# Performance work log

Measured on AMD Instinct MI355X. Metric: run time of the kernel, lower is better.

Reference implementation:

```python
import jax, jax.numpy as jnp
import numpy as np

BN_EPS = 1e-5
KEEP_RATIO = 0.25
MIN_TOPK = 4


def setup_inputs() -> dict:
    key = jax.random.key(0)
    ks = jax.random.split(key, 8)
    B, C, H, W, HID = 32, 768, 32, 32, 96
    x = jax.random.normal(ks[0], (B, C, H, W), dtype=jnp.float32)
    # fan-in scaled weights so score magnitudes stay sane for softmax
    w1 = jax.random.normal(ks[1], (HID, C, 1, 1), dtype=jnp.float32) / np.sqrt(C)
    bn_gamma = jax.random.uniform(ks[2], (HID,), dtype=jnp.float32) + 0.5
    bn_beta = jax.random.normal(ks[3], (HID,), dtype=jnp.float32) * 0.1
    bn_mean = jax.random.normal(ks[4], (HID,), dtype=jnp.float32) * 0.1
    bn_var = jax.random.uniform(ks[5], (HID,), dtype=jnp.float32) + 0.5
    w2 = jax.random.normal(ks[6], (1, HID, 3, 3), dtype=jnp.float32) / np.sqrt(HID * 9)
    b2 = jax.random.normal(ks[7], (1,), dtype=jnp.float32) * 0.1
    return {"x": x, "w1": w1, "bn_gamma": bn_gamma, "bn_beta": bn_beta,
            "bn_mean": bn_mean, "bn_var": bn_var, "w2": w2, "b2": b2}


def reference(x, w1, bn_gamma, bn_beta, bn_mean, bn_var, w2, b2):
    B, C, H, W = x.shape
    N = H * W
    # 1x1 conv (no bias) as channel contraction: [B,C,H,W] x [HID,C] -> [B,HID,H,W]
    h = jnp.einsum('bchw,oc->bohw', x, w1[:, :, 0, 0])
    # BatchNorm in inference mode (running stats)
    scale = (bn_gamma / jnp.sqrt(bn_var + BN_EPS))[None, :, None, None]
    h = h * scale + (bn_beta - bn_mean * bn_gamma / jnp.sqrt(bn_var + BN_EPS))[None, :, None, None]
    h = jax.nn.relu(h)
    # 3x3 conv HID -> 1, padding=1
    score = jax.lax.conv_general_dilated(
        h, w2, window_strides=(1, 1), padding='SAME',
        dimension_numbers=('NCHW', 'OIHW', 'NCHW')) + b2[None, :, None, None]
    s = score.reshape(B, N)
    K = min(max(MIN_TOPK, int(N * KEEP_RATIO)), N)
    top_vals, top_idx = jax.lax.top_k(s, K)  # [B,K] (sorted; weighted sum is order-invariant)
    x_flat = x.reshape(B, C, N)
    sel = jnp.take_along_axis(x_flat, top_idx[:, None, :], axis=2)  # [B,C,K]
    w = jax.nn.softmax(top_vals, axis=1)[:, None, :]               # [B,1,K]
    v = jnp.sum(sel * w, axis=2)                                    # [B,C]
    # dropout p=0.0 -> identity
    return v, score.reshape(B, 1, H, W)
```

## Files before the change

### kernel.cpp

```cpp
#include <hip/hip_runtime.h>
#include <math.h>

#define BB 32
#define CC 768
#define HID 96
#define NPIX 1024
#define KSEL 256
#define BN_EPS_F 1e-5f

typedef __bf16 bf16x8 __attribute__((ext_vector_type(8)));
typedef float f32x4 __attribute__((ext_vector_type(4)));

__device__ __forceinline__ unsigned short f2bf(float f) {
    unsigned u = __float_as_uint(f);
    return (unsigned short)((u + 0x7FFFu + ((u >> 16) & 1u)) >> 16);
}
__device__ __forceinline__ unsigned pack2(float lo, float hi) {
    return (unsigned)f2bf(lo) | ((unsigned)f2bf(hi) << 16);
}

__global__ __launch_bounds__(512, 4) void k1_gemm_mfma(
    const float* __restrict__ x, const float* __restrict__ w1,
    const float* __restrict__ gamma, const float* __restrict__ beta,
    const float* __restrict__ mean, const float* __restrict__ var,
    float* __restrict__ h_out)
{
    constexpr int WSTR = 388;
    __shared__ unsigned short Ws[96 * WSTR];
    __shared__ float sc_s[HID], sh_s[HID];

    const int t = threadIdx.x;
    const int b = blockIdx.y;
    const int n0 = blockIdx.x * 64;
    const int wave = t >> 6, lane = t & 63;
    const int lm = lane & 15, g = lane >> 4;
    const int wo = wave & 1, wn = wave >> 1;
    const int n = n0 + wn * 16 + lm;

    if (t < HID) {
        float sc = gamma[t] * rsqrtf(var[t] + BN_EPS_F);
        sc_s[t] = sc;
        sh_s[t] = beta[t] - mean[t] * sc;
    }

    f32x4 acc[3];
#pragma unroll
    for (int mt = 0; mt < 3; ++mt) acc[mt] = (f32x4){0.f, 0.f, 0.f, 0.f};

    const float* xcol = x + (size_t)b * CC * NPIX + (size_t)(g * 8) * NPIX + n;

#define STAGE_W(half) do {                                                    \
    _Pragma("unroll")                                                         \
    for (int i = 0; i < 9; ++i) {                                             \
        int idx = t + i * 512;                                   \
        int row = idx / 48, k8 = (idx % 48) * 8;                              \
        const float* src = w1 + (size_t)row * CC + (half) * 384 + k8;         \
        float4 f0 = *reinterpret_cast<const float4*>(src);                    \
        float4 f1 = *reinterpret_cast<const float4*>(src + 4);                \
        uint4 o;                                                              \
        o.x = pack2(f0.x, f0.y); o.y = pack2(f0.z, f0.w);                     \
        o.z = pack2(f1.x, f1.y); o.w = pack2(f1.z, f1.w);                     \
        *reinterpret_cast<uint4*>(&Ws[row * WSTR + k8]) = o;                  \
    } } while (0)

#define LOADX(dst, ck) do {                                                   \
    const float* _p = xcol + (size_t)(ck) * 32 * NPIX;                        \
    _Pragma("unroll")                                                         \
    for (int j = 0; j < 8; ++j) dst[j] = _p[(size_t)j * NPIX];                \
    } while (0)

#define PACKX(bu, src) do {                                                   \
    bu.x = pack2(src[0], src[1]); bu.y = pack2(src[2], src[3]);               \
    bu.z = pack2(src[4], src[5]); bu.w = pack2(src[6], src[7]); } while (0)

#define CHUNK(ckk, bu) do {                                                   \
    bf16x8 bfr = __builtin_bit_cast(bf16x8, bu);                              \
    _Pragma("unroll")                                                         \
    for (int mt = 0; mt < 3; ++mt) {                                          \
        uint4 au = *reinterpret_cast<const uint4*>(                           \
            &Ws[(wo * 48 + mt * 16 + lm) * WSTR + (ckk) * 32 + g * 8]);       \
        acc[mt] = __builtin_amdgcn_mfma_f32_16x16x32_bf16(                    \
            __builtin_bit_cast(bf16x8, au), bfr, acc[mt], 0, 0, 0);           \
    } } while (0)

    float xA[8], xB[8], xC[8], xD[8];

    STAGE_W(0);
    LOADX(xA, 0); LOADX(xB, 1); LOADX(xC, 2); LOADX(xD, 3);
    __syncthreads();

#pragma unroll
    for (int ck = 0; ck < 24; ck += 4) {
        if (ck == 12) {
            __syncthreads();
            STAGE_W(1);
            __syncthreads();
        }
        uint4 bu0; PACKX(bu0, xA);
        if (ck + 4 < 24) LOADX(xA, ck + 4);
        CHUNK((ck + 0) % 12, bu0);

        uint4 bu1; PACKX(bu1, xB);
        if (ck + 5 < 24) LOADX(xB, ck + 5);
        CHUNK((ck + 1) % 12, bu1);

        uint4 bu2; PACKX(bu2, xC);
        if (ck + 6 < 24) LOADX(xC, ck + 6);
        CHUNK((ck + 2) % 12, bu2);

        uint4 bu3; PACKX(bu3, xD);
        if (ck + 7 < 24) LOADX(xD, ck + 7);
        CHUNK((ck + 3) % 12, bu3);
    }

#pragma unroll
    for (int mt = 0; mt < 3; ++mt) {
#pragma unroll
        for (int r = 0; r < 4; ++r) {
            int o = wo * 48 + mt * 16 + g * 4 + r;
            float v = fmaxf(acc[mt][r] * sc_s[o] + sh_s[o], 0.f);
            h_out[((size_t)b * HID + o) * NPIX + n] = v;
        }
    }
#undef STAGE_W
#undef LOADX
#undef PACKX
#undef CHUNK
}

__global__ __launch_bounds__(128) void k2_conv3x3(
    const float* __restrict__ h_in, const float* __restrict__ w2,
    const float* __restrict__ b2, float* __restrict__ score_out)
{
    __shared__ float hs[16][6][40];
    __shared__ float w2s[HID * 9];

    const int t = threadIdx.x;
    const int ytile = blockIdx.x, b = blockIdx.y;
    const int y = t >> 5, xx = t & 31;
    const int Y = ytile * 4 + y;

    for (int i = t; i < HID * 9; i += 128) w2s[i] = w2[i];

    const float* hb = h_in + (size_t)b * HID * NPIX;
    float acc = 0.f;

    for (int c0 = 0; c0 < HID; c0 += 16) {
        __syncthreads();
        for (int i = t; i < 192; i += 128) {
            int ch = i / 12, rr = (i % 12) >> 1, col = (i & 1) ? 36 : 3;
            hs[ch][rr][col] = 0.f;
        }
#pragma unroll
        for (int i = 0; i < 6; ++i) {
            int idx = t + i * 128;
            int ch = idx / 48, rem = idx % 48;
            int rr = rem >> 3, qq = rem & 7;
            int gy = ytile * 4 - 1 + rr;
            float4 v = (gy >= 0 && gy < 32)
                ? *reinterpret_cast<const float4*>(
                      hb + (size_t)(c0 + ch) * NPIX + gy * 32 + qq * 4)
                : (float4){0.f, 0.f, 0.f, 0.f};
            *reinterpret_cast<float4*>(&hs[ch][rr][4 + qq * 4]) = v;
        }
        __syncthreads();
#pragma unroll
        for (int ch = 0; ch < 16; ++ch) {
            float s = 0.f;
#pragma unroll
            for (int ky = 0; ky < 3; ++ky)
#pragma unroll
                for (int kx = 0; kx < 3; ++kx)
                    s += hs[ch][y + ky][3 + xx + kx] * w2s[(c0 + ch) * 9 + ky * 3 + kx];
            acc += s;
        }
    }
    score_out[b * NPIX + Y * 32 + xx] = acc + b2[0];
}

__global__ __launch_bounds__(256) void k3_topk_softmax(
    const float* __restrict__ score, float* __restrict__ weight)
{
    __shared__ unsigned hist[256];
    __shared__ unsigned wtot[4];
    __shared__ unsigned pcnt16[16];
    __shared__ float redf[4];
    __shared__ unsigned sh_bin, sh_rem;

    const int t = threadIdx.x, b = blockIdx.x;
    const int lane = t & 63, wv = t >> 6;

    float fvals[4];
    unsigned uvals[4];
#pragma unroll
    for (int i = 0; i < 4; ++i) {
        float f = score[b * NPIX + t + 256 * i];
        fvals[i] = f;
        unsigned u = __float_as_uint(f);
        uvals[i] = (u & 0x80000000u) ? ~u : (u | 0x80000000u);
    }

    unsigned prefix = 0, rem = KSEL;
    for (int p = 3; p >= 0; --p) {
        hist[t] = 0;
        __syncthreads();
        const int sh_hi = (p + 1) * 8;
#pragma unroll
        for (int i = 0; i < 4; ++i) {
            unsigned u = uvals[i];
            bool match = (p == 3) || ((u >> sh_hi) == (prefix >> sh_hi));
            if (match) atomicAdd(&hist[(u >> (p * 8)) & 0xffu], 1u);
        }
        __syncthreads();
        unsigned own = hist[t];
        unsigned val = own;
#pragma unroll
        for (int off = 1; off <= 32; off <<= 1) {
            unsigned o2 = __shfl_down(val, off);
            if (lane + off < 64) val += o2;
        }
        if (lane == 0) wtot[wv] = val;
        __syncthreads();
        unsigned suff = val;
        for (int w = wv + 1; w < 4; ++w) suff += wtot[w];
        unsigned nexts = suff - own;
        if (suff >= rem && nexts < rem) { sh_bin = (unsigned)t; sh_rem = rem - nexts; }
        __syncthreads();
        prefix |= (sh_bin << (p * 8));
        rem = sh_rem;
        __syncthreads();
    }
    const unsigned T = prefix, need = rem;

    float m = -INFINITY;
#pragma unroll
    for (int i = 0; i < 4; ++i) m = fmaxf(m, fvals[i]);
#pragma unroll
    for (int off = 32; off >= 1; off >>= 1) m = fmaxf(m, __shfl_xor(m, off));
    if (lane == 0) redf[wv] = m;
    __syncthreads();
    m = fmaxf(fmaxf(redf[0], redf[1]), fmaxf(redf[2], redf[3]));

    unsigned lp[4]; bool eqf[4], gtf[4];
    unsigned long long lmask = (1ULL << lane) - 1ULL;
#pragma unroll
    for (int i = 0; i < 4; ++i) {
        bool eq = (uvals[i] == T);
        eqf[i] = eq; gtf[i] = (uvals[i] > T);
        unsigned long long mk = __ballot(eq);
        lp[i] = (unsigned)__popcll(mk & lmask);
        if (lane == 0) pcnt16[i * 4 + wv] = (unsigned)__popcll(mk);
    }
    __syncthreads();
    unsigned cum = 0, baseArr[4];
#pragma unroll
    for (int ii = 0; ii < 4; ++ii) {
        unsigned b0 = cum;
        for (int w = 0; w < wv; ++w) b0 += pcnt16[ii * 4 + w];
        baseArr[ii] = b0;
        for (int w = 0; w < 4; ++w) cum += pcnt16[ii * 4 + w];
    }
    float evals[4], sumExp = 0.f;
#pragma unroll
    for (int i = 0; i < 4; ++i) {
        bool sel = gtf[i] || (eqf[i] && (baseArr[i] + lp[i]) < need);
        float e = sel ? expf(fvals[i] - m) : 0.f;
        evals[i] = e;
        sumExp += e;
    }
#pragma unroll
    for (int off = 32; off >= 1; off >>= 1) sumExp += __shfl_xor(sumExp, off);
    if (lane == 0) redf[wv] = sumExp;
    __syncthreads();
    float inv = 1.0f / (redf[0] + redf[1] + redf[2] + redf[3]);
#pragma unroll
    for (int i = 0; i < 4; ++i)
        weight[b * NPIX + i * 256 + t] = evals[i] * inv;
}

__global__ __launch_bounds__(256) void k4_weighted_sum(
    const float* __restrict__ x, const float* __restrict__ weight,
    float* __restrict__ v)
{
    __shared__ float wsm[NPIX];
    const int t = threadIdx.x;
    const int b = blockIdx.x / 192, cg = blockIdx.x % 192;

    *reinterpret_cast<float4*>(&wsm[t * 4]) =
        *reinterpret_cast<const float4*>(&weight[b * NPIX + t * 4]);
    __syncthreads();

    const int lane = t & 63, wvv = t >> 6;
    const int c = cg * 4 + wvv;
    const float* xr = x + ((size_t)b * CC + c) * NPIX;

    float acc = 0.f;
#pragma unroll
    for (int j = 0; j < 4; ++j) {
        int off = j * 256 + lane * 4;
        float4 xv = *reinterpret_cast<const float4*>(xr + off);
        float4 wv4 = *reinterpret_cast<const float4*>(&wsm[off]);
        acc += xv.x * wv4.x + xv.y * wv4.y + xv.z * wv4.z + xv.w * wv4.w;
    }
#pragma unroll
    for (int off = 32; off >= 1; off >>= 1) acc += __shfl_xor(acc, off);
    if (lane == 0) v[(size_t)b * CC + c] = acc;
}

extern "C" void kernel_launch(void* const* d_in, const int* in_sizes, int n_in,
                              void* d_out, int out_size, void* d_ws, size_t ws_size,
                              hipStream_t stream)
{
    const float* x     = (const float*)d_in[0];
    const float* w1    = (const float*)d_in[1];
    const float* gamma = (const float*)d_in[2];
    const float* beta  = (const float*)d_in[3];
    const float* mean  = (const float*)d_in[4];
    const float* var   = (const float*)d_in[5];
    const float* w2    = (const float*)d_in[6];
    const float* b2    = (const float*)d_in[7];

    float* out   = (float*)d_out;
    float* vout  = out;
    float* score = out + BB * CC;

    float* h      = (float*)d_ws;
    float* weight = h + (size_t)BB * HID * NPIX;

    k1_gemm_mfma<<<dim3(16, BB), 512, 0, stream>>>(x, w1, gamma, beta, mean, var, h);
    k2_conv3x3<<<dim3(8, BB), 128, 0, stream>>>(h, w2, b2, score);
    k3_topk_softmax<<<BB, 256, 0, stream>>>(score, weight);
    k4_weighted_sum<<<BB * (CC / 4), 256, 0, stream>>>(x, weight, vout);
}
```

Measured before the change: 74.43 us.

## Widen GEMM tile to 128 pixels with float2 x loads and dual MFMA accumulators

The 1x1-conv GEMM kernel now covers 128 pixels per block instead of 64. Each lane loads adjacent pixel pairs as float2 and feeds two MFMA accumulator sets, so every bf16 weight fragment read from shared memory is reused twice. This halves the number of blocks and the redundant staging of W1 into LDS per block, and widens the global loads and stores. In exchange it uses more registers per thread, lowers the launch-bounds occupancy hint from 4 to 2, and leaves fewer blocks (256) to spread across the CUs.

```diff
diff --git a/kernel.cpp b/kernel.cpp
--- a/kernel.cpp
+++ b/kernel.cpp
@@ -19,7 +19,7 @@
     return (unsigned)f2bf(lo) | ((unsigned)f2bf(hi) << 16);
 }
 
-__global__ __launch_bounds__(512, 4) void k1_gemm_mfma(
+__global__ __launch_bounds__(512, 2) void k1_gemm_mfma(
     const float* __restrict__ x, const float* __restrict__ w1,
     const float* __restrict__ gamma, const float* __restrict__ beta,
     const float* __restrict__ mean, const float* __restrict__ var,
@@ -31,11 +31,12 @@
 
     const int t = threadIdx.x;
     const int b = blockIdx.y;
-    const int n0 = blockIdx.x * 64;
+    const int n0 = blockIdx.x * 128;
     const int wave = t >> 6, lane = t & 63;
     const int lm = lane & 15, g = lane >> 4;
-    const int wo = wave & 1, wn = wave >> 1;
-    const int n = n0 + wn * 16 + lm;
+    const int wo = wave >> 2, wn = wave & 3;
+    const int nw = n0 + wn * 32;
+    const int ncol = nw + 2 * lm;
 
     if (t < HID) {
         float sc = gamma[t] * rsqrtf(var[t] + BN_EPS_F);
@@ -43,11 +44,14 @@
         sh_s[t] = beta[t] - mean[t] * sc;
     }
 
-    f32x4 acc[3];
-#pragma unroll
-    for (int mt = 0; mt < 3; ++mt) acc[mt] = (f32x4){0.f, 0.f, 0.f, 0.f};
-
-    const float* xcol = x + (size_t)b * CC * NPIX + (size_t)(g * 8) * NPIX + n;
+    f32x4 acc0[3], acc1[3];
+#pragma unroll
+    for (int mt = 0; mt < 3; ++mt) {
+        acc0[mt] = (f32x4){0.f, 0.f, 0.f, 0.f};
+        acc1[mt] = (f32x4){0.f, 0.f, 0.f, 0.f};
+    }
+
+    const float* xcol = x + (size_t)b * CC * NPIX + (size_t)(g * 8) * NPIX + ncol;
 
 #define STAGE_W(half) do {                                                    \
     _Pragma("unroll")                                                         \
@@ -66,24 +70,32 @@
 #define LOADX(dst, ck) do {                                                   \
     const float* _p = xcol + (size_t)(ck) * 32 * NPIX;                        \
     _Pragma("unroll")                                                         \
-    for (int j = 0; j < 8; ++j) dst[j] = _p[(size_t)j * NPIX];                \
+    for (int j = 0; j < 8; ++j)                                               \
+        dst[j] = *reinterpret_cast<const float2*>(_p + (size_t)j * NPIX);     \
     } while (0)
 
-#define PACKX(bu, src) do {                                                   \
-    bu.x = pack2(src[0], src[1]); bu.y = pack2(src[2], src[3]);               \
-    bu.z = pack2(src[4], src[5]); bu.w = pack2(src[6], src[7]); } while (0)
-
-#define CHUNK(ckk, bu) do {                                                   \
-    bf16x8 bfr = __builtin_bit_cast(bf16x8, bu);                              \
+#define PACKX(bu0, bu1, src) do {                                             \
+    bu0.x = pack2(src[0].x, src[1].x); bu0.y = pack2(src[2].x, src[3].x);     \
+    bu0.z = pack2(src[4].x, src[5].x); bu0.w = pack2(src[6].x, src[7].x);     \
+    bu1.x = pack2(src[0].y, src[1].y); bu1.y = pack2(src[2].y, src[3].y);     \
+    bu1.z = pack2(src[4].y, src[5].y); bu1.w = pack2(src[6].y, src[7].y);     \
+    } while (0)
+
+#define CHUNK(ckk, bu0, bu1) do {                                             \
+    bf16x8 bf0 = __builtin_bit_cast(bf16x8, bu0);                             \
+    bf16x8 bf1 = __builtin_bit_cast(bf16x8, bu1);                             \
     _Pragma("unroll")                                                         \
     for (int mt = 0; mt < 3; ++mt) {                                          \
         uint4 au = *reinterpret_cast<const uint4*>(                           \
             &Ws[(wo * 48 + mt * 16 + lm) * WSTR + (ckk) * 32 + g * 8]);       \
-        acc[mt] = __builtin_amdgcn_mfma_f32_16x16x32_bf16(                    \
-            __builtin_bit_cast(bf16x8, au), bfr, acc[mt], 0, 0, 0);           \
+        bf16x8 abf = __builtin_bit_cast(bf16x8, au);                          \
+        acc0[mt] = __builtin_amdgcn_mfma_f32_16x16x32_bf16(                   \
+            abf, bf0, acc0[mt], 0, 0, 0);                                     \
+        acc1[mt] = __builtin_amdgcn_mfma_f32_16x16x32_bf16(                   \
+            abf, bf1, acc1[mt], 0, 0, 0);                                     \
     } } while (0)
 
-    float xA[8], xB[8], xC[8], xD[8];
+    float2 xA[8], xB[8], xC[8], xD[8];
 
     STAGE_W(0);
     LOADX(xA, 0); LOADX(xB, 1); LOADX(xC, 2); LOADX(xD, 3);
@@ -96,21 +108,25 @@
             STAGE_W(1);
             __syncthreads();
         }
-        uint4 bu0; PACKX(bu0, xA);
+        uint4 p0, p1;
+        PACKX(p0, p1, xA);
         if (ck + 4 < 24) LOADX(xA, ck + 4);
-        CHUNK((ck + 0) % 12, bu0);
-
-        uint4 bu1; PACKX(bu1, xB);
+        CHUNK((ck + 0) % 12, p0, p1);
+
+        uint4 q0, q1;
+        PACKX(q0, q1, xB);
         if (ck + 5 < 24) LOADX(xB, ck + 5);
-        CHUNK((ck + 1) % 12, bu1);
-
-        uint4 bu2; PACKX(bu2, xC);
+        CHUNK((ck + 1) % 12, q0, q1);
+
+        uint4 r0, r1;
+        PACKX(r0, r1, xC);
         if (ck + 6 < 24) LOADX(xC, ck + 6);
-        CHUNK((ck + 2) % 12, bu2);
-
-        uint4 bu3; PACKX(bu3, xD);
+        CHUNK((ck + 2) % 12, r0, r1);
+
+        uint4 s0, s1;
+        PACKX(s0, s1, xD);
         if (ck + 7 < 24) LOADX(xD, ck + 7);
-        CHUNK((ck + 3) % 12, bu3);
+        CHUNK((ck + 3) % 12, s0, s1);
     }
 
 #pragma unroll
@@ -118,8 +134,12 @@
 #pragma unroll
         for (int r = 0; r < 4; ++r) {
             int o = wo * 48 + mt * 16 + g * 4 + r;
-            float v = fmaxf(acc[mt][r] * sc_s[o] + sh_s[o], 0.f);
-            h_out[((size_t)b * HID + o) * NPIX + n] = v;
+            float sc = sc_s[o], sh = sh_s[o];
+            float2 v;
+            v.x = fmaxf(acc0[mt][r] * sc + sh, 0.f);
+            v.y = fmaxf(acc1[mt][r] * sc + sh, 0.f);
+            *reinterpret_cast<float2*>(
+                &h_out[((size_t)b * HID + o) * NPIX + ncol]) = v;
         }
     }
 #undef STAGE_W
@@ -327,7 +347,7 @@
     float* h      = (float*)d_ws;
     float* weight = h + (size_t)BB * HID * NPIX;
 
-    k1_gemm_mfma<<<dim3(16, BB), 512, 0, stream>>>(x, w1, gamma, beta, mean, var, h);
+    k1_gemm_mfma<<<dim3(8, BB), 512, 0, stream>>>(x, w1, gamma, beta, mean, var, h);
     k2_conv3x3<<<dim3(8, BB), 128, 0, stream>>>(h, w2, b2, score);
     k3_topk_softmax<<<BB, 256, 0, stream>>>(score, weight);
     k4_weighted_sum<<<BB * (CC / 4), 256, 0, stream>>>(x, weight, vout);
```

Result: slower. 75.94 us (+2.0%).

## Split GEMM K dimension across two blocks and precompute bf16 weights

Applied to the files above, without the earlier changes.

Adds a prep kernel that converts w1 to bf16 once and computes BN scale/shift. The 1x1-conv GEMM is split into two K halves across a grid z dimension, each writing a partial result. The BN, ReLU and partial-sum reduction move into the conv3x3 load stage, and shared memory per GEMM block shrinks to allow higher occupancy. The aim is more parallelism and less per-block weight staging, at the cost of an extra kernel launch and twice the intermediate h traffic.

```diff
diff --git a/kernel.cpp b/kernel.cpp
--- a/kernel.cpp
+++ b/kernel.cpp
@@ -19,121 +19,126 @@
     return (unsigned)f2bf(lo) | ((unsigned)f2bf(hi) << 16);
 }
 
-__global__ __launch_bounds__(512, 4) void k1_gemm_mfma(
-    const float* __restrict__ x, const float* __restrict__ w1,
-    const float* __restrict__ gamma, const float* __restrict__ beta,
-    const float* __restrict__ mean, const float* __restrict__ var,
-    float* __restrict__ h_out)
-{
-    constexpr int WSTR = 388;
-    __shared__ unsigned short Ws[96 * WSTR];
-    __shared__ float sc_s[HID], sh_s[HID];
+__global__ __launch_bounds__(256) void k0_prep(
+    const float* __restrict__ w1, const float* __restrict__ gamma,
+    const float* __restrict__ beta, const float* __restrict__ mean,
+    const float* __restrict__ var,
+    unsigned short* __restrict__ w1b, float* __restrict__ scale,
+    float* __restrict__ shift)
+{
+    int t = threadIdx.x, bk = blockIdx.x;
+    if (bk < 72) {
+        int idx = (bk * 256 + t) * 4;
+        float4 v = *reinterpret_cast<const float4*>(w1 + idx);
+        uint2 o;
+        o.x = pack2(v.x, v.y);
+        o.y = pack2(v.z, v.w);
+        *reinterpret_cast<uint2*>(w1b + idx) = o;
+    } else if (t < HID) {
+        float sc = gamma[t] * rsqrtf(var[t] + BN_EPS_F);
+        scale[t] = sc;
+        shift[t] = beta[t] - mean[t] * sc;
+    }
+}
+
+__global__ __launch_bounds__(512, 6) void k1_gemm_mfma(
+    const float* __restrict__ x, const unsigned short* __restrict__ w1b,
+    float* __restrict__ h0, float* __restrict__ h1)
+{
+    __shared__ unsigned short Ws[96][100];
 
     const int t = threadIdx.x;
     const int b = blockIdx.y;
     const int n0 = blockIdx.x * 64;
+    const int kz = blockIdx.z;
+    const int kbase = kz * 384;
     const int wave = t >> 6, lane = t & 63;
     const int lm = lane & 15, g = lane >> 4;
-    const int wo = wave & 1, wn = wave >> 1;
+    const int wo = wave >> 2, wn = wave & 3;
     const int n = n0 + wn * 16 + lm;
 
-    if (t < HID) {
-        float sc = gamma[t] * rsqrtf(var[t] + BN_EPS_F);
-        sc_s[t] = sc;
-        sh_s[t] = beta[t] - mean[t] * sc;
-    }
-
     f32x4 acc[3];
 #pragma unroll
     for (int mt = 0; mt < 3; ++mt) acc[mt] = (f32x4){0.f, 0.f, 0.f, 0.f};
 
-    const float* xcol = x + (size_t)b * CC * NPIX + (size_t)(g * 8) * NPIX + n;
-
-#define STAGE_W(half) do {                                                    \
+    const float* xcol = x + (size_t)b * CC * NPIX
+                          + (size_t)(kbase + g * 8) * NPIX + n;
+
+#define STAGE_W(e) do {                                                       \
+    for (int ii = t; ii < 1152; ii += 512) {                                  \
+        int row = ii / 12, kc = (ii % 12) * 8;                                \
+        uint4 wv = *reinterpret_cast<const uint4*>(                           \
+            w1b + (size_t)row * CC + kbase + (e) * 96 + kc);                  \
+        *reinterpret_cast<uint4*>(&Ws[row][kc]) = wv;                         \
+    } } while (0)
+
+#define LOADX(dst, s) do {                                                    \
     _Pragma("unroll")                                                         \
-    for (int i = 0; i < 9; ++i) {                                             \
-        int idx = t + i * 512;                                   \
-        int row = idx / 48, k8 = (idx % 48) * 8;                              \
-        const float* src = w1 + (size_t)row * CC + (half) * 384 + k8;         \
-        float4 f0 = *reinterpret_cast<const float4*>(src);                    \
-        float4 f1 = *reinterpret_cast<const float4*>(src + 4);                \
-        uint4 o;                                                              \
-        o.x = pack2(f0.x, f0.y); o.y = pack2(f0.z, f0.w);                     \
-        o.z = pack2(f1.x, f1.y); o.w = pack2(f1.z, f1.w);                     \
-        *reinterpret_cast<uint4*>(&Ws[row * WSTR + k8]) = o;                  \
-    } } while (0)
-
-#define LOADX(dst, ck) do {                                                   \
-    const float* _p = xcol + (size_t)(ck) * 32 * NPIX;                        \
-    _Pragma("unroll")                                                         \
-    for (int j = 0; j < 8; ++j) dst[j] = _p[(size_t)j * NPIX];                \
+    for (int j = 0; j < 8; ++j)                                               \
+        dst[j] = xcol[(size_t)((s) * 32 + j) * NPIX];                         \
     } while (0)
 
 #define PACKX(bu, src) do {                                                   \
     bu.x = pack2(src[0], src[1]); bu.y = pack2(src[2], src[3]);               \
     bu.z = pack2(src[4], src[5]); bu.w = pack2(src[6], src[7]); } while (0)
 
-#define CHUNK(ckk, bu) do {                                                   \
+#define DOCHUNK(sl, bu) do {                                                  \
     bf16x8 bfr = __builtin_bit_cast(bf16x8, bu);                              \
     _Pragma("unroll")                                                         \
     for (int mt = 0; mt < 3; ++mt) {                                          \
         uint4 au = *reinterpret_cast<const uint4*>(                           \
-            &Ws[(wo * 48 + mt * 16 + lm) * WSTR + (ckk) * 32 + g * 8]);       \
+            &Ws[wo * 48 + mt * 16 + lm][(sl) * 32 + g * 8]);                  \
         acc[mt] = __builtin_amdgcn_mfma_f32_16x16x32_bf16(                    \
             __builtin_bit_cast(bf16x8, au), bfr, acc[mt], 0, 0, 0);           \
     } } while (0)
 
-    float xA[8], xB[8], xC[8], xD[8];
+#define STEP(sc, CUR) do {                                                    \
+    uint4 bu;                                                                 \
+    PACKX(bu, CUR);                                                           \
+    if ((sc) + 2 < 12) LOADX(CUR, (sc) + 2);                                  \
+    DOCHUNK((sc) % 3, bu);                                                    \
+    } while (0)
+
+    float xA[8], xB[8];
 
     STAGE_W(0);
-    LOADX(xA, 0); LOADX(xB, 1); LOADX(xC, 2); LOADX(xD, 3);
-    __syncthreads();
-
-#pragma unroll
-    for (int ck = 0; ck < 24; ck += 4) {
-        if (ck == 12) {
-            __syncthreads();
-            STAGE_W(1);
-            __syncthreads();
-        }
-        uint4 bu0; PACKX(bu0, xA);
-        if (ck + 4 < 24) LOADX(xA, ck + 4);
-        CHUNK((ck + 0) % 12, bu0);
-
-        uint4 bu1; PACKX(bu1, xB);
-        if (ck + 5 < 24) LOADX(xB, ck + 5);
-        CHUNK((ck + 1) % 12, bu1);
-
-        uint4 bu2; PACKX(bu2, xC);
-        if (ck + 6 < 24) LOADX(xC, ck + 6);
-        CHUNK((ck + 2) % 12, bu2);
-
-        uint4 bu3; PACKX(bu3, xD);
-        if (ck + 7 < 24) LOADX(xD, ck + 7);
-        CHUNK((ck + 3) % 12, bu3);
-    }
-
+    LOADX(xA, 0);
+    LOADX(xB, 1);
+    __syncthreads();
+
+    STEP(0, xA); STEP(1, xB); STEP(2, xA);
+    __syncthreads(); STAGE_W(1); __syncthreads();
+    STEP(3, xB); STEP(4, xA); STEP(5, xB);
+    __syncthreads(); STAGE_W(2); __syncthreads();
+    STEP(6, xA); STEP(7, xB); STEP(8, xA);
+    __syncthreads(); STAGE_W(3); __syncthreads();
+    STEP(9, xB); STEP(10, xA); STEP(11, xB);
+
+    float* hp = (kz == 0) ? h0 : h1;
 #pragma unroll
     for (int mt = 0; mt < 3; ++mt) {
 #pragma unroll
         for (int r = 0; r < 4; ++r) {
             int o = wo * 48 + mt * 16 + g * 4 + r;
-            float v = fmaxf(acc[mt][r] * sc_s[o] + sh_s[o], 0.f);
-            h_out[((size_t)b * HID + o) * NPIX + n] = v;
+            hp[((size_t)b * HID + o) * NPIX + n] = acc[mt][r];
         }
     }
 #undef STAGE_W
 #undef LOADX
 #undef PACKX
-#undef CHUNK
+#undef DOCHUNK
+#undef STEP
 }
 
 __global__ __launch_bounds__(128) void k2_conv3x3(
-    const float* __restrict__ h_in, const float* __restrict__ w2,
-    const float* __restrict__ b2, float* __restrict__ score_out)
+    const float* __restrict__ h0, const float* __restrict__ h1,
+    const float* __restrict__ scale, const float* __restrict__ shift,
+    const float* __restrict__ w2, const float* __restrict__ b2,
+    float* __restrict__ score_out)
 {
     __shared__ float hs[16][6][40];
     __shared__ float w2s[HID * 9];
+    __shared__ float sc_s[HID], sh_s[HID];
 
     const int t = threadIdx.x;
     const int ytile = blockIdx.x, b = blockIdx.y;
@@ -141,8 +146,10 @@
     const int Y = ytile * 4 + y;
 
     for (int i = t; i < HID * 9; i += 128) w2s[i] = w2[i];
-
-    const float* hb = h_in + (size_t)b * HID * NPIX;
+    if (t < HID) { sc_s[t] = scale[t]; sh_s[t] = shift[t]; }
+
+    const float* hb0 = h0 + (size_t)b * HID * NPIX;
+    const float* hb1 = h1 + (size_t)b * HID * NPIX;
     float acc = 0.f;
 
     for (int c0 = 0; c0 < HID; c0 += 16) {
@@ -157,10 +164,17 @@
             int ch = idx / 48, rem = idx % 48;
             int rr = rem >> 3, qq = rem & 7;
             int gy = ytile * 4 - 1 + rr;
-            float4 v = (gy >= 0 && gy < 32)
-                ? *reinterpret_cast<const float4*>(
-                      hb + (size_t)(c0 + ch) * NPIX + gy * 32 + qq * 4)
-                : (float4){0.f, 0.f, 0.f, 0.f};
+            float4 v = {0.f, 0.f, 0.f, 0.f};
+            if (gy >= 0 && gy < 32) {
+                size_t off = (size_t)(c0 + ch) * NPIX + gy * 32 + qq * 4;
+                float4 a = *reinterpret_cast<const float4*>(hb0 + off);
+                float4 c = *reinterpret_cast<const float4*>(hb1 + off);
+                float sc = sc_s[c0 + ch], sh = sh_s[c0 + ch];
+                v.x = fmaxf((a.x + c.x) * sc + sh, 0.f);
+                v.y = fmaxf((a.y + c.y) * sc + sh, 0.f);
+                v.z = fmaxf((a.z + c.z) * sc + sh, 0.f);
+                v.w = fmaxf((a.w + c.w) * sc + sh, 0.f);
+            }
             *reinterpret_cast<float4*>(&hs[ch][rr][4 + qq * 4]) = v;
         }
         __syncthreads();
@@ -324,11 +338,16 @@
     float* vout  = out;
     float* score = out + BB * CC;
 
-    float* h      = (float*)d_ws;
-    float* weight = h + (size_t)BB * HID * NPIX;
-
-    k1_gemm_mfma<<<dim3(16, BB), 512, 0, stream>>>(x, w1, gamma, beta, mean, var, h);
-    k2_conv3x3<<<dim3(8, BB), 128, 0, stream>>>(h, w2, b2, score);
+    float* h0      = (float*)d_ws;
+    float* h1      = h0 + (size_t)BB * HID * NPIX;
+    float* weight  = h1 + (size_t)BB * HID * NPIX;
+    unsigned short* w1b = (unsigned short*)(weight + BB * NPIX);
+    float* scale   = (float*)(w1b + HID * CC);
+    float* shift   = scale + HID;
+
+    k0_prep<<<73, 256, 0, stream>>>(w1, gamma, beta, mean, var, w1b, scale, shift);
+    k1_gemm_mfma<<<dim3(16, BB, 2), 512, 0, stream>>>(x, w1b, h0, h1);
+    k2_conv3x3<<<dim3(8, BB), 128, 0, stream>>>(h0, h1, scale, shift, w2, b2, score);
     k3_topk_softmax<<<BB, 256, 0, stream>>>(score, weight);
     k4_weighted_sum<<<BB * (CC / 4), 256, 0, stream>>>(x, weight, vout);
 }
```

New measurement: 80.58 us. +8.3%, slower.

## Pre-transpose x to bf16 pixel-major and pre-convert weights before GEMM

Applied to the files above, without the earlier changes.

Adds a transpose kernel that converts x to bf16 in a [B, N, C] layout, plus a prep kernel that converts w1 to bf16 and precomputes the BatchNorm scale and shift. The GEMM can then load 16-byte contiguous bf16 B-fragments instead of eight strided fp32 loads followed by packing. The wave-to-tile mapping also changes. In exchange, there is an extra full pass over x: it reads the fp32 tensor and writes a bf16 copy into the workspace, which the GEMM then reads back. That adds memory traffic and two more launches to a pipeline that is already memory-bound.

```diff
diff --git a/kernel.cpp b/kernel.cpp
--- a/kernel.cpp
+++ b/kernel.cpp
@@ -19,10 +19,75 @@
     return (unsigned)f2bf(lo) | ((unsigned)f2bf(hi) << 16);
 }
 
-__global__ __launch_bounds__(512, 4) void k1_gemm_mfma(
-    const float* __restrict__ x, const float* __restrict__ w1,
-    const float* __restrict__ gamma, const float* __restrict__ beta,
-    const float* __restrict__ mean, const float* __restrict__ var,
+__global__ __launch_bounds__(256) void k0_prep(
+    const float* __restrict__ w1, const float* __restrict__ gamma,
+    const float* __restrict__ beta, const float* __restrict__ mean,
+    const float* __restrict__ var,
+    unsigned short* __restrict__ w1b, float* __restrict__ scale,
+    float* __restrict__ shift)
+{
+    int t = threadIdx.x, bk = blockIdx.x;
+    if (bk < 72) {
+        int idx = (bk * 256 + t) * 4;
+        float4 v = *reinterpret_cast<const float4*>(w1 + idx);
+        uint2 o;
+        o.x = pack2(v.x, v.y);
+        o.y = pack2(v.z, v.w);
+        *reinterpret_cast<uint2*>(w1b + idx) = o;
+    } else if (t < HID) {
+        float sc = gamma[t] * rsqrtf(var[t] + BN_EPS_F);
+        scale[t] = sc;
+        shift[t] = beta[t] - mean[t] * sc;
+    }
+}
+
+__global__ __launch_bounds__(256) void kP_transpose(
+    const float* __restrict__ x, unsigned short* __restrict__ xt)
+{
+    __shared__ unsigned Lu[32 * 517];
+
+    const int t = threadIdx.x;
+    const int c0 = blockIdx.x * 32, b = blockIdx.y;
+
+#pragma unroll
+    for (int p = 0; p < 4; ++p) {
+        int r = p * 8 + (t >> 5);
+        int seg = t & 31;
+        const float* src = x + ((size_t)b * CC + c0 + r) * NPIX + seg * 32;
+        unsigned* dst = &Lu[r * 517 + seg * 16];
+#pragma unroll
+        for (int j = 0; j < 8; ++j) {
+            float4 v = *reinterpret_cast<const float4*>(src + 4 * j);
+            dst[2 * j]     = pack2(v.x, v.y);
+            dst[2 * j + 1] = pack2(v.z, v.w);
+        }
+    }
+    __syncthreads();
+
+    const int l4 = t & 3;
+    const int nq = t >> 2;
+#pragma unroll 4
+    for (int it = 0; it < 16; ++it) {
+        int n = it * 64 + nq;
+        unsigned ou[4];
+#pragma unroll
+        for (int i2 = 0; i2 < 4; ++i2) {
+            int cl0 = l4 * 8 + 2 * i2;
+            unsigned a = Lu[cl0 * 517 + (n >> 1)];
+            unsigned c = Lu[(cl0 + 1) * 517 + (n >> 1)];
+            unsigned sa = (n & 1) ? (a >> 16) : (a & 0xffffu);
+            unsigned sc = (n & 1) ? (c >> 16) : (c & 0xffffu);
+            ou[i2] = sa | (sc << 16);
+        }
+        uint4 o4 = {ou[0], ou[1], ou[2], ou[3]};
+        *reinterpret_cast<uint4*>(
+            xt + ((size_t)b * NPIX + n) * CC + c0 + l4 * 8) = o4;
+    }
+}
+
+__global__ __launch_bounds__(512) void k1_gemm_mfma(
+    const unsigned short* __restrict__ xt, const unsigned short* __restrict__ w1b,
+    const float* __restrict__ scale, const float* __restrict__ shift,
     float* __restrict__ h_out)
 {
     constexpr int WSTR = 388;
@@ -34,46 +99,32 @@
     const int n0 = blockIdx.x * 64;
     const int wave = t >> 6, lane = t & 63;
     const int lm = lane & 15, g = lane >> 4;
-    const int wo = wave & 1, wn = wave >> 1;
+    const int wo = wave >> 2, wn = wave & 3;
     const int n = n0 + wn * 16 + lm;
 
-    if (t < HID) {
-        float sc = gamma[t] * rsqrtf(var[t] + BN_EPS_F);
-        sc_s[t] = sc;
-        sh_s[t] = beta[t] - mean[t] * sc;
-    }
+    if (t < HID) { sc_s[t] = scale[t]; sh_s[t] = shift[t]; }
 
     f32x4 acc[3];
 #pragma unroll
     for (int mt = 0; mt < 3; ++mt) acc[mt] = (f32x4){0.f, 0.f, 0.f, 0.f};
 
-    const float* xcol = x + (size_t)b * CC * NPIX + (size_t)(g * 8) * NPIX + n;
+    const unsigned short* xrow = xt + ((size_t)b * NPIX + n) * CC + g * 8;
 
 #define STAGE_W(half) do {                                                    \
     _Pragma("unroll")                                                         \
     for (int i = 0; i < 9; ++i) {                                             \
         int idx = t + i * 512;                                   \
         int row = idx / 48, k8 = (idx % 48) * 8;                              \
-        const float* src = w1 + (size_t)row * CC + (half) * 384 + k8;         \
-        float4 f0 = *reinterpret_cast<const float4*>(src);                    \
-        float4 f1 = *reinterpret_cast<const float4*>(src + 4);                \
-        uint4 o;                                                              \
-        o.x = pack2(f0.x, f0.y); o.y = pack2(f0.z, f0.w);                     \
-        o.z = pack2(f1.x, f1.y); o.w = pack2(f1.z, f1.w);                     \
-        *reinterpret_cast<uint4*>(&Ws[row * WSTR + k8]) = o;                  \
+        uint4 wv = *reinterpret_cast<const uint4*>(                           \
+            w1b + (size_t)row * CC + (half) * 384 + k8);                      \
+        *reinterpret_cast<uint4*>(&Ws[row * WSTR + k8]) = wv;                 \
     } } while (0)
 
-#define LOADX(dst, ck) do {                                                   \
-    const float* _p = xcol + (size_t)(ck) * 32 * NPIX;                        \
-    _Pragma("unroll")                                                         \
-    for (int j = 0; j < 8; ++j) dst[j] = _p[(size_t)j * NPIX];                \
+#define LOADB(dst, ck) do {                                                   \
+    dst = *reinterpret_cast<const uint4*>(xrow + (size_t)(ck) * 32);          \
     } while (0)
 
-#define PACKX(bu, src) do {                                                   \
-    bu.x = pack2(src[0], src[1]); bu.y = pack2(src[2], src[3]);               \
-    bu.z = pack2(src[4], src[5]); bu.w = pack2(src[6], src[7]); } while (0)
-
-#define CHUNK(ckk, bu) do {                                                   \
+#define DOCHUNK(ckk, bu) do {                                                 \
     bf16x8 bfr = __builtin_bit_cast(bf16x8, bu);                              \
     _Pragma("unroll")                                                         \
     for (int mt = 0; mt < 3; ++mt) {                                          \
@@ -83,35 +134,27 @@
             __builtin_bit_cast(bf16x8, au), bfr, acc[mt], 0, 0, 0);           \
     } } while (0)
 
-    float xA[8], xB[8], xC[8], xD[8];
+#define STEP(ck, SLOT) do {                                                   \
+    uint4 bu = SLOT;                                                          \
+    if ((ck) + 4 < 24) LOADB(SLOT, (ck) + 4);                                 \
+    DOCHUNK((ck) % 12, bu);                                                   \
+    } while (0)
+
+    uint4 x0, x1, x2, x3;
 
     STAGE_W(0);
-    LOADX(xA, 0); LOADX(xB, 1); LOADX(xC, 2); LOADX(xD, 3);
-    __syncthreads();
-
-#pragma unroll
-    for (int ck = 0; ck < 24; ck += 4) {
-        if (ck == 12) {
-            __syncthreads();
-            STAGE_W(1);
-            __syncthreads();
-        }
-        uint4 bu0; PACKX(bu0, xA);
-        if (ck + 4 < 24) LOADX(xA, ck + 4);
-        CHUNK((ck + 0) % 12, bu0);
-
-        uint4 bu1; PACKX(bu1, xB);
-        if (ck + 5 < 24) LOADX(xB, ck + 5);
-        CHUNK((ck + 1) % 12, bu1);
-
-        uint4 bu2; PACKX(bu2, xC);
-        if (ck + 6 < 24) LOADX(xC, ck + 6);
-        CHUNK((ck + 2) % 12, bu2);
-
-        uint4 bu3; PACKX(bu3, xD);
-        if (ck + 7 < 24) LOADX(xD, ck + 7);
-        CHUNK((ck + 3) % 12, bu3);
-    }
+    LOADB(x0, 0); LOADB(x1, 1); LOADB(x2, 2); LOADB(x3, 3);
+    __syncthreads();
+
+    STEP(0, x0);  STEP(1, x1);  STEP(2, x2);  STEP(3, x3);
+    STEP(4, x0);  STEP(5, x1);  STEP(6, x2);  STEP(7, x3);
+    STEP(8, x0);  STEP(9, x1);  STEP(10, x2); STEP(11, x3);
+    __syncthreads();
+    STAGE_W(1);
+    __syncthreads();
+    STEP(12, x0); STEP(13, x1); STEP(14, x2); STEP(15, x3);
+    STEP(16, x0); STEP(17, x1); STEP(18, x2); STEP(19, x3);
+    STEP(20, x0); STEP(21, x1); STEP(22, x2); STEP(23, x3);
 
 #pragma unroll
     for (int mt = 0; mt < 3; ++mt) {
@@ -123,9 +166,9 @@
         }
     }
 #undef STAGE_W
-#undef LOADX
-#undef PACKX
-#undef CHUNK
+#undef LOADB
+#undef DOCHUNK
+#undef STEP
 }
 
 __global__ __launch_bounds__(128) void k2_conv3x3(
@@ -324,10 +367,16 @@
     float* vout  = out;
     float* score = out + BB * CC;
 
-    float* h      = (float*)d_ws;
+    unsigned short* xt = (unsigned short*)d_ws;
+    float* h      = (float*)(xt + (size_t)BB * NPIX * CC);
     float* weight = h + (size_t)BB * HID * NPIX;
-
-    k1_gemm_mfma<<<dim3(16, BB), 512, 0, stream>>>(x, w1, gamma, beta, mean, var, h);
+    unsigned short* w1b = (unsigned short*)(weight + BB * NPIX);
+    float* scale  = (float*)(w1b + HID * CC);
+    float* shift  = scale + HID;
+
+    k0_prep<<<73, 256, 0, stream>>>(w1, gamma, beta, mean, var, w1b, scale, shift);
+    kP_transpose<<<dim3(24, BB), 256, 0, stream>>>(x, xt);
+    k1_gemm_mfma<<<dim3(16, BB), 512, 0, stream>>>(xt, w1b, scale, shift, h);
     k2_conv3x3<<<dim3(8, BB), 128, 0, stream>>>(h, w2, b2, score);
     k3_topk_softmax<<<BB, 256, 0, stream>>>(score, weight);
     k4_weighted_sum<<<BB * (CC / 4), 256, 0, stream>>>(x, weight, vout);
```

Result: slower. 116.5 us (+56.5%).
